# Kernel tuning notes

Hardware: AMD Instinct MI355X
Metric: run time of the kernel (lower is better)

The kernel has to match this reference:

```python
import jax, jax.numpy as jnp
import numpy as np

N = 400_000            # nodes
E = 8_000_000          # edges (avg degree 20)
USER, TOPIC, CAT, GROUP = 200_000, 50_000, 2_000, 30_000
UD, TD, CD, GD = 8, 8, 2, 8   # embedding dims
C = 8                  # input_channels
H = 16                 # hidden layer width
OUT = 1


def setup_inputs() -> dict:
    key = jax.random.key(0)
    ks = jax.random.split(key, 24)

    # node types in {0:user, 1:topic, 2:category, 4:group}
    t = jnp.take(jnp.array([0, 1, 2, 4], dtype=jnp.int32),
                 jax.random.randint(ks[0], (N,), 0, 4))
    # per-type vocab sizes (index 3 is an unused dummy)
    vocab = jnp.array([USER, TOPIC, CAT, 1, GROUP], dtype=jnp.int32)[t]
    i0 = jax.random.randint(ks[1], (N,), 0, 1 << 30) % vocab
    i1 = jax.random.randint(ks[2], (N,), 0, 2)  # known-user flag
    features = jnp.stack([i0, i1, t], axis=1)            # [N, 3] int32
    edges = jax.random.randint(ks[3], (2, E), 0, N)      # [2, E]

    g = lambda k, shape: 0.02 * jax.random.normal(k, shape, dtype=jnp.float32)
    return {
        "edges": edges,
        "features": features,
        "user_emb": g(ks[4], (USER, UD)),
        "known_emb": g(ks[5], (2, UD)),
        "Wu": g(ks[6], (UD, C)), "bu": g(ks[7], (C,)),
        "topic_emb": g(ks[8], (TOPIC, TD)),
        "Wt": g(ks[9], (TD, C)), "bt": g(ks[10], (C,)),
        "cat_emb": g(ks[11], (CAT, CD)),
        "Wc": g(ks[12], (CD, C)), "bc": g(ks[13], (C,)),
        "group_emb": g(ks[14], (GROUP, GD)),
        "Wg": g(ks[15], (GD, C)), "bg": g(ks[16], (C,)),
        "W0": g(ks[17], (C, H)), "b0": g(ks[18], (H,)),
        "W2": g(ks[19], (H, OUT)), "b2": g(ks[20], (OUT,)),
    }


def reference(edges, features, user_emb, known_emb, Wu, bu,
              topic_emb, Wt, bt, cat_emb, Wc, bc,
              group_emb, Wg, bg, W0, b0, W2, b2):
    t = features[:, -1]
    i0 = features[:, 0]
    i1 = features[:, 1]

    # type-specific embedding gather + ReLU + linear projection (safe-indexed)
    u = jax.nn.relu(user_emb[jnp.where(t == 0, i0, 0)]
                    + known_emb[jnp.where(t == 0, i1, 0)]) @ Wu + bu
    tp = jax.nn.relu(topic_emb[jnp.where(t == 1, i0, 0)]) @ Wt + bt
    c = jax.nn.relu(cat_emb[jnp.where(t == 2, i0, 0)]) @ Wc + bc
    g = jax.nn.relu(group_emb[jnp.where(t == 4, i0, 0)]) @ Wg + bg

    tc = t[:, None]
    x = (jnp.where(tc == 0, u, 0.0) + jnp.where(tc == 1, tp, 0.0)
         + jnp.where(tc == 2, c, 0.0) + jnp.where(tc == 4, g, 0.0))  # [N, C]

    n = x.shape[0]
    loops = jnp.arange(n, dtype=edges.dtype)
    row = jnp.concatenate([edges[0], loops])   # source (with self loops)
    col = jnp.concatenate([edges[1], loops])   # target
    deg = jax.ops.segment_sum(jnp.ones_like(col, dtype=x.dtype), col,
                              num_segments=n)
    dinv = jnp.where(deg > 0, jax.lax.rsqrt(deg), 0.0)
    norm = dinv[row] * dinv[col]               # [E+N]

    def gcn_conv(h, W, b):  # PyG GCNConv: D^-1/2 (A+I) D^-1/2 h W + b
        hw = h @ W
        agg = jax.ops.segment_sum(norm[:, None] * hw[row], col, num_segments=n)
        return agg + b

    # original forward applies layers[0] (+ReLU) then layers[-1];
    # the middle GCNConv is skipped and dropout never fires.
    h = jax.nn.relu(gcn_conv(x, W0, b0))
    return gcn_conv(h, W2, b2)
```

## Files before the change

### kernel.cpp

```cpp
#include <hip/hip_runtime.h>

#define SH 10
#define BN 1024
#define CAP 22016
#define TILE 4096
#define MAXB 512
#define NCH 8
#define CSH 16
#define AGG_NB 1024


__device__ __forceinline__ unsigned short f2bf(float f) {
    union { float f; unsigned u; } x; x.f = f;
    unsigned u = x.u + 0x7fffu + ((x.u >> 16) & 1u);
    return (unsigned short)(u >> 16);
}
__device__ __forceinline__ float u2f(unsigned u) {
    union { unsigned u; float f; } x; x.u = u;
    return x.f;
}


__global__ void k_binit(int* __restrict__ bcursor, int pbkt) {
    int b = blockIdx.x * blockDim.x + threadIdx.x;
    if (b < pbkt) bcursor[b] = b * CAP;
}

__global__ void __launch_bounds__(256)
k_part(const int* __restrict__ row, const int* __restrict__ col,
       int* __restrict__ bcursor, unsigned* __restrict__ ebuf, int e) {
    __shared__ int lcnt[MAXB];
    __shared__ int gbase[MAXB];
    int t = threadIdx.x;
    int base = blockIdx.x * TILE;
    for (int j = t; j < MAXB; j += 256) lcnt[j] = 0;
    __syncthreads();
    int myb[16]; int mylpos[16]; unsigned myv[16];
#pragma unroll
    for (int k = 0; k < 16; k++) {
        int i = base + k * 256 + t;
        if (i < e) {
            int r = row[i];
            int c = col[i];
            int b = c >> SH;
            myb[k] = b;
            myv[k] = ((unsigned)r << SH) | (unsigned)(c & (BN - 1));
            mylpos[k] = atomicAdd(&lcnt[b], 1);
        } else {
            myb[k] = -1;
        }
    }
    __syncthreads();
    for (int j = t; j < MAXB; j += 256)
        if (lcnt[j] > 0) gbase[j] = atomicAdd(&bcursor[j], lcnt[j]);
    __syncthreads();
#pragma unroll
    for (int k = 0; k < 16; k++) {
        if (myb[k] >= 0) {
            int idx = gbase[myb[k]] + mylpos[k];
            if (idx < (myb[k] + 1) * CAP) ebuf[idx] = myv[k];
        }
    }
}

__global__ void k_bscan(const int* __restrict__ bcursor, int* __restrict__ bbase, int bkt) {
    __shared__ int sd[256];
    int t = threadIdx.x;
    int i0 = t * 2, i1 = t * 2 + 1;
    int v0 = (i0 < bkt) ? (bcursor[i0] - i0 * CAP) : 0;
    int v1 = (i1 < bkt) ? (bcursor[i1] - i1 * CAP) : 0;
    int s = v0 + v1;
    sd[t] = s; __syncthreads();
    for (int off = 1; off < 256; off <<= 1) {
        int x = (t >= off) ? sd[t - off] : 0;
        __syncthreads();
        sd[t] += x;
        __syncthreads();
    }
    int run = sd[t] - s;
    if (i0 < bkt) bbase[i0] = run;
    if (i1 < bkt) bbase[i1] = run + v0;
}


__global__ void __launch_bounds__(512)
k_scatB(const int* __restrict__ bcursor, const int* __restrict__ bbase,
        const unsigned* __restrict__ ebuf, int* __restrict__ csr,
        int* __restrict__ start, int* __restrict__ cnt, float* __restrict__ dinv,
        uint2* __restrict__ chunkCnt, int n, int bkt) {
    __shared__ int lcnt[BN * NCH];
    __shared__ unsigned stage[CAP];
    __shared__ int sd[512];
    int b = blockIdx.x;
    if (b >= bkt) return;
    int t = threadIdx.x;
    int ebase = b * CAP;
    int len = bcursor[b] - ebase;
    if (len > CAP) len = CAP;
    int cbase = bbase[b];

    for (int j = t; j < BN * NCH; j += 512) lcnt[j] = 0;
    __syncthreads();
    for (int i = t; i < len; i += 512) {
        unsigned vv = ebuf[ebase + i];
        int bin = (int)((vv & (BN - 1)) << 3) | (int)((vv >> SH) >> CSH);
        atomicAdd(&lcnt[bin], 1);
    }
    __syncthreads();
    int v[16]; int s = 0;
#pragma unroll
    for (int k = 0; k < 16; k++) { v[k] = lcnt[t * 16 + k]; s += v[k]; }
    sd[t] = s; __syncthreads();
    for (int off = 1; off < 512; off <<= 1) {
        int x = (t >= off) ? sd[t - off] : 0;
        __syncthreads();
        sd[t] += x;
        __syncthreads();
    }
    int run = sd[t] - s;
    int node0 = b << SH;
#pragma unroll
    for (int nn = 0; nn < 2; nn++) {
        int node = node0 + t * 2 + nn;
        int segbase = run;
        unsigned packA = 0, packB = 0;
        int tot = 0;
#pragma unroll
        for (int k2 = 0; k2 < 8; k2++) {
            int cc = v[nn * 8 + k2];
            lcnt[t * 16 + nn * 8 + k2] = run;
            run += cc; tot += cc;
            unsigned ccs = (unsigned)(cc > 255 ? 255 : cc);
            if (k2 < 4) packA |= ccs << (8 * k2);
            else        packB |= ccs << (8 * (k2 - 4));
        }
        if (node < n) {
            start[node] = cbase + segbase;
            cnt[node] = tot;
            dinv[node] = rsqrtf((float)tot + 1.0f);
            chunkCnt[node] = make_uint2(packA, packB);
        }
    }
    __syncthreads();
    for (int i = t; i < len; i += 512) {
        unsigned vv = ebuf[ebase + i];
        unsigned r = vv >> SH;
        int bin = (int)((vv & (BN - 1)) << 3) | (int)(r >> CSH);
        int p = atomicAdd(&lcnt[bin], 1);
        if (p < CAP) stage[p] = r;
        else csr[cbase + p] = (int)r;
    }
    __syncthreads();
    for (int j = t; j < len; j += 512) csr[cbase + j] = (int)stage[j];
}


__device__ __forceinline__ void matvec8(const float* e, const float* W, const float* b, float* x) {
#pragma unroll
    for (int c = 0; c < 8; c++) x[c] = b[c];
#pragma unroll
    for (int k = 0; k < 8; k++) {
        float r = fmaxf(e[k], 0.0f);
#pragma unroll
        for (int c = 0; c < 8; c++) x[c] = fmaf(r, W[k * 8 + c], x[c]);
    }
}

__global__ void __launch_bounds__(256)
k_node(const int* __restrict__ feat,
       const float* __restrict__ user_emb, const float* __restrict__ known_emb,
       const float* __restrict__ Wu, const float* __restrict__ bu,
       const float* __restrict__ topic_emb, const float* __restrict__ Wt, const float* __restrict__ bt,
       const float* __restrict__ cat_emb, const float* __restrict__ Wc, const float* __restrict__ bc,
       const float* __restrict__ group_emb, const float* __restrict__ Wg, const float* __restrict__ bg,
       const float* __restrict__ W0, const float* __restrict__ dinv,
       unsigned short* __restrict__ yb, int n) {
    __shared__ float sWu[64], sWt[64], sWc[64], sWg[64];
    __shared__ float sbu[8], sbt[8], sbc[8], sbg[8];
    __shared__ float sW0[128];
    int t = threadIdx.x;
    if (t < 64) {
        sWu[t] = Wu[t];
        sWt[t] = Wt[t];
        sWc[t] = (t < 16) ? Wc[t] : 0.0f;
        sWg[t] = Wg[t];
    } else if (t < 192) {
        sW0[t - 64] = W0[t - 64];
    } else if (t < 200) {
        int k = t - 192;
        sbu[k] = bu[k]; sbt[k] = bt[k]; sbc[k] = bc[k]; sbg[k] = bg[k];
    }
    __syncthreads();

    int i = blockIdx.x * blockDim.x + t;
    if (i >= n) return;

    int i0 = feat[3 * i + 0];
    int i1 = feat[3 * i + 1];
    int ty = feat[3 * i + 2];

    float x[8];
    float e[8];
    if (ty == 0) {
        const float4* u = (const float4*)(user_emb + (size_t)i0 * 8);
        const float4* kn = (const float4*)(known_emb + (size_t)i1 * 8);
        float4 a0 = u[0], a1 = u[1], k0 = kn[0], k1 = kn[1];
        e[0] = a0.x + k0.x; e[1] = a0.y + k0.y; e[2] = a0.z + k0.z; e[3] = a0.w + k0.w;
        e[4] = a1.x + k1.x; e[5] = a1.y + k1.y; e[6] = a1.z + k1.z; e[7] = a1.w + k1.w;
        matvec8(e, sWu, sbu, x);
    } else if (ty == 1) {
        const float4* u = (const float4*)(topic_emb + (size_t)i0 * 8);
        float4 a0 = u[0], a1 = u[1];
        e[0] = a0.x; e[1] = a0.y; e[2] = a0.z; e[3] = a0.w;
        e[4] = a1.x; e[5] = a1.y; e[6] = a1.z; e[7] = a1.w;
        matvec8(e, sWt, sbt, x);
    } else if (ty == 2) {
        const float2* u = (const float2*)(cat_emb + (size_t)i0 * 2);
        float2 a = u[0];
        e[0] = a.x; e[1] = a.y;
#pragma unroll
        for (int k = 2; k < 8; k++) e[k] = 0.0f;
        matvec8(e, sWc, sbc, x);
    } else if (ty == 4) {
        const float4* u = (const float4*)(group_emb + (size_t)i0 * 8);
        float4 a0 = u[0], a1 = u[1];
        e[0] = a0.x; e[1] = a0.y; e[2] = a0.z; e[3] = a0.w;
        e[4] = a1.x; e[5] = a1.y; e[6] = a1.z; e[7] = a1.w;
        matvec8(e, sWg, sbg, x);
    } else {
#pragma unroll
        for (int c = 0; c < 8; c++) x[c] = 0.0f;
    }

    float di = dinv[i];
    float yv[16];
#pragma unroll
    for (int h = 0; h < 16; h++) {
        float acc = 0.0f;
#pragma unroll
        for (int c = 0; c < 8; c++) acc = fmaf(x[c], sW0[c * 16 + h], acc);
        yv[h] = di * acc;
    }
    unsigned p[8];
#pragma unroll
    for (int k = 0; k < 8; k++)
        p[k] = (unsigned)f2bf(yv[2 * k]) | ((unsigned)f2bf(yv[2 * k + 1]) << 16);
    uint4* o = (uint4*)(yb + (size_t)i * 16);
    o[0] = make_uint4(p[0], p[1], p[2], p[3]);
    o[1] = make_uint4(p[4], p[5], p[6], p[7]);
}


__device__ __forceinline__ void upadd(uint4 v, float* a) {
    a[0] += u2f(v.x << 16); a[1] += u2f(v.x & 0xffff0000u);
    a[2] += u2f(v.y << 16); a[3] += u2f(v.y & 0xffff0000u);
    a[4] += u2f(v.z << 16); a[5] += u2f(v.z & 0xffff0000u);
    a[6] += u2f(v.w << 16); a[7] += u2f(v.w & 0xffff0000u);
}

__global__ void __launch_bounds__(256, 4)
k_agg1(const int* __restrict__ start, const uint2* __restrict__ chunkCnt,
       const int* __restrict__ csr, const uint4* __restrict__ y4,
       const float* __restrict__ dinv, const float* __restrict__ b0,
       const float* __restrict__ W2, float* __restrict__ y2, int n, int nPerBlk) {
    int t = threadIdx.x;
    int j = t & 1;
    int p = t >> 1;
    int base = blockIdx.x * nPerBlk;
    int end = base + nPerBlk; if (end > n) end = n;

    float acc[4][8];
    int cur[4]; int nd[4];
    unsigned cc0[4], cc1[4];
#pragma unroll
    for (int k = 0; k < 4; k++) {
        int node = base + p + k * 128;
        nd[k] = node;
#pragma unroll
        for (int ch = 0; ch < 8; ch++) acc[k][ch] = 0.0f;
        if (node < end) {
            cur[k] = start[node];
            uint2 cc = chunkCnt[node];
            cc0[k] = cc.x; cc1[k] = cc.y;
            upadd(y4[(size_t)node * 2 + j], acc[k]);
        } else {
            cur[k] = 0; cc0[k] = 0; cc1[k] = 0;
        }
    }

    for (int c = 0; c < 7; c++) {
        int sh = (c & 3) * 8;
#pragma unroll
        for (int k = 0; k < 4; k++) {
            unsigned packed = (c < 4) ? cc0[k] : cc1[k];
            int cc = (int)((packed >> sh) & 255u);
            int s = cur[k];
            cur[k] = s + cc;
            int i = 0;
            for (; i + 2 <= cc; i += 2) {
                int r0 = csr[s + i];
                int r1 = csr[s + i + 1];
                uint4 v0 = y4[(size_t)r0 * 2 + j];
                uint4 v1 = y4[(size_t)r1 * 2 + j];
                upadd(v0, acc[k]); upadd(v1, acc[k]);
            }
            if (i < cc) upadd(y4[(size_t)csr[s + i] * 2 + j], acc[k]);
        }
    }

    float4 bA = ((const float4*)b0)[2 * j];
    float4 bB = ((const float4*)b0)[2 * j + 1];
    float4 wA = ((const float4*)W2)[2 * j];
    float4 wB = ((const float4*)W2)[2 * j + 1];
#pragma unroll
    for (int k = 0; k < 4; k++) {
        if (nd[k] >= end) continue;
        float di = dinv[nd[k]];
        float v = 0.0f;
        v += fmaxf(fmaf(acc[k][0], di, bA.x), 0.0f) * wA.x;
        v += fmaxf(fmaf(acc[k][1], di, bA.y), 0.0f) * wA.y;
        v += fmaxf(fmaf(acc[k][2], di, bA.z), 0.0f) * wA.z;
        v += fmaxf(fmaf(acc[k][3], di, bA.w), 0.0f) * wA.w;
        v += fmaxf(fmaf(acc[k][4], di, bB.x), 0.0f) * wB.x;
        v += fmaxf(fmaf(acc[k][5], di, bB.y), 0.0f) * wB.y;
        v += fmaxf(fmaf(acc[k][6], di, bB.z), 0.0f) * wB.z;
        v += fmaxf(fmaf(acc[k][7], di, bB.w), 0.0f) * wB.w;
        v += __shfl_xor(v, 1);
        if (j == 0) y2[nd[k]] = di * v;
    }
}

__global__ void __launch_bounds__(256)
k_agg2(const int* __restrict__ start, const int* __restrict__ cnt,
       const int* __restrict__ csr, const float* __restrict__ y2,
       const float* __restrict__ dinv, const float* __restrict__ b2,
       float* __restrict__ out, int n) {
    int gid = blockIdx.x * blockDim.x + threadIdx.x;
    int node = gid >> 2;
    int j = gid & 3;
    if (node >= n) return;
    int s = start[node];
    int d = cnt[node];
    float acc = (j == 0) ? y2[node] : 0.0f;
    for (int i = j; i < d; i += 4) acc += y2[csr[s + i]];
    acc += __shfl_xor(acc, 1);
    acc += __shfl_xor(acc, 2);
    if (j == 0) out[node] = fmaf(acc, dinv[node], b2[0]);
}


static inline size_t align_up(size_t v, size_t a) { return (v + a - 1) & ~(a - 1); }

extern "C" void kernel_launch(void* const* d_in, const int* in_sizes, int n_in,
                              void* d_out, int out_size, void* d_ws, size_t ws_size,
                              hipStream_t stream) {
    const int E = in_sizes[0] / 2;
    const int N = in_sizes[1] / 3;

    const int* edges    = (const int*)d_in[0];
    const int* row      = edges;
    const int* col      = edges + E;
    const int* feat     = (const int*)d_in[1];
    const float* user_emb  = (const float*)d_in[2];
    const float* known_emb = (const float*)d_in[3];
    const float* Wu = (const float*)d_in[4];
    const float* bu = (const float*)d_in[5];
    const float* topic_emb = (const float*)d_in[6];
    const float* Wt = (const float*)d_in[7];
    const float* bt = (const float*)d_in[8];
    const float* cat_emb = (const float*)d_in[9];
    const float* Wc = (const float*)d_in[10];
    const float* bc = (const float*)d_in[11];
    const float* group_emb = (const float*)d_in[12];
    const float* Wg = (const float*)d_in[13];
    const float* bg = (const float*)d_in[14];
    const float* W0 = (const float*)d_in[15];
    const float* b0 = (const float*)d_in[16];
    const float* W2 = (const float*)d_in[17];
    const float* b2 = (const float*)d_in[18];

    float* out = (float*)d_out;

    const int BKT  = (N + BN - 1) >> SH;
    const int PBKT = (BKT + 7) & ~7;

    char* w = (char*)d_ws;
    size_t off = 0;
    int* cnt      = (int*)(w + off); off = align_up(off + (size_t)N * 4, 256);
    int* start    = (int*)(w + off); off = align_up(off + (size_t)N * 4, 256);
    float* dinv   = (float*)(w + off); off = align_up(off + (size_t)N * 4, 256);
    float* y2     = (float*)(w + off); off = align_up(off + (size_t)N * 4, 256);
    uint2* chunkCnt = (uint2*)(w + off); off = align_up(off + (size_t)N * 8, 256);
    int* bcursor  = (int*)(w + off); off = align_up(off + MAXB * 4, 256);
    int* bbase    = (int*)(w + off); off = align_up(off + MAXB * 4, 256);
    size_t bigsz = (size_t)BKT * CAP * 4;
    if ((size_t)N * 32 > bigsz) bigsz = (size_t)N * 32;
    unsigned* ebuf      = (unsigned*)(w + off);
    unsigned short* yb  = (unsigned short*)(w + off); off = align_up(off + bigsz, 256);
    int* csr      = (int*)(w + off); off = align_up(off + (size_t)E * 4, 256);
    (void)ws_size;

    int tb = 256;
    int gbN = (N + tb - 1) / tb;
    int ntile = (E + TILE - 1) / TILE;

    k_binit<<<(PBKT + 255) / 256, 256, 0, stream>>>(bcursor, PBKT);
    k_part<<<ntile, tb, 0, stream>>>(row, col, bcursor, ebuf, E);
    k_bscan<<<1, 256, 0, stream>>>(bcursor, bbase, BKT);
    k_scatB<<<BKT, 512, 0, stream>>>(bcursor, bbase, ebuf, csr, start, cnt, dinv,
                                     chunkCnt, N, BKT);
    k_node<<<gbN, tb, 0, stream>>>(feat, user_emb, known_emb, Wu, bu,
                                   topic_emb, Wt, bt, cat_emb, Wc, bc,
                                   group_emb, Wg, bg, W0, dinv, yb, N);
    int nPerBlk = (N + AGG_NB - 1) / AGG_NB;
    k_agg1<<<AGG_NB, tb, 0, stream>>>(start, chunkCnt, csr, (const uint4*)yb,
                                      dinv, b0, W2, y2, N, nPerBlk);
    int gbA24 = ((N * 4) + tb - 1) / tb;
    k_agg2<<<gbA24, tb, 0, stream>>>(start, cnt, csr, y2, dinv, b2, out, N);
}
```

Baseline: 289.3 us.

## Compress CSR source indices to 16-bit offsets within per-chunk ranges

```diff
diff --git a/kernel.cpp b/kernel.cpp
--- a/kernel.cpp
+++ b/kernel.cpp
@@ -7,7 +7,6 @@
 #define MAXB 512
 #define NCH 8
 #define CSH 16
-#define AGG_NB 1024
 
 
 __device__ __forceinline__ unsigned short f2bf(float f) {
@@ -83,13 +82,13 @@
 }
 
 
-__global__ void __launch_bounds__(512)
+__global__ void __launch_bounds__(512, 4)
 k_scatB(const int* __restrict__ bcursor, const int* __restrict__ bbase,
-        const unsigned* __restrict__ ebuf, int* __restrict__ csr,
-        int* __restrict__ start, int* __restrict__ cnt, float* __restrict__ dinv,
+        const unsigned* __restrict__ ebuf, unsigned short* __restrict__ csr16,
+        int* __restrict__ start, float* __restrict__ dinv,
         uint2* __restrict__ chunkCnt, int n, int bkt) {
     __shared__ int lcnt[BN * NCH];
-    __shared__ unsigned stage[CAP];
+    __shared__ unsigned short stage[CAP];
     __shared__ int sd[512];
     int b = blockIdx.x;
     if (b >= bkt) return;
@@ -136,7 +135,6 @@
         }
         if (node < n) {
             start[node] = cbase + segbase;
-            cnt[node] = tot;
             dinv[node] = rsqrtf((float)tot + 1.0f);
             chunkCnt[node] = make_uint2(packA, packB);
         }
@@ -147,11 +145,12 @@
         unsigned r = vv >> SH;
         int bin = (int)((vv & (BN - 1)) << 3) | (int)(r >> CSH);
         int p = atomicAdd(&lcnt[bin], 1);
-        if (p < CAP) stage[p] = r;
-        else csr[cbase + p] = (int)r;
-    }
-    __syncthreads();
-    for (int j = t; j < len; j += 512) csr[cbase + j] = (int)stage[j];
+        unsigned short off16 = (unsigned short)(r & 0xFFFFu);
+        if (p < CAP) stage[p] = off16;
+        else csr16[cbase + p] = off16;
+    }
+    __syncthreads();
+    for (int j = t; j < len; j += 512) csr16[cbase + j] = stage[j];
 }
 
 
@@ -258,93 +257,92 @@
     a[6] += u2f(v.w << 16); a[7] += u2f(v.w & 0xffff0000u);
 }
 
-__global__ void __launch_bounds__(256, 4)
+__global__ void __launch_bounds__(256, 8)
 k_agg1(const int* __restrict__ start, const uint2* __restrict__ chunkCnt,
-       const int* __restrict__ csr, const uint4* __restrict__ y4,
+       const unsigned short* __restrict__ csr16, const uint4* __restrict__ y4,
        const float* __restrict__ dinv, const float* __restrict__ b0,
-       const float* __restrict__ W2, float* __restrict__ y2, int n, int nPerBlk) {
-    int t = threadIdx.x;
-    int j = t & 1;
-    int p = t >> 1;
-    int base = blockIdx.x * nPerBlk;
-    int end = base + nPerBlk; if (end > n) end = n;
-
-    float acc[4][8];
-    int cur[4]; int nd[4];
-    unsigned cc0[4], cc1[4];
-#pragma unroll
-    for (int k = 0; k < 4; k++) {
-        int node = base + p + k * 128;
-        nd[k] = node;
-#pragma unroll
-        for (int ch = 0; ch < 8; ch++) acc[k][ch] = 0.0f;
-        if (node < end) {
-            cur[k] = start[node];
-            uint2 cc = chunkCnt[node];
-            cc0[k] = cc.x; cc1[k] = cc.y;
-            upadd(y4[(size_t)node * 2 + j], acc[k]);
-        } else {
-            cur[k] = 0; cc0[k] = 0; cc1[k] = 0;
-        }
-    }
-
+       const float* __restrict__ W2, float* __restrict__ y2, int n) {
+    int node = blockIdx.x * 256 + threadIdx.x;
+    bool act = node < n;
+    float acc[16];
+#pragma unroll
+    for (int k = 0; k < 16; k++) acc[k] = 0.0f;
+    int cur = 0;
+    uint2 cc = make_uint2(0u, 0u);
+    if (act) {
+        cur = start[node];
+        cc = chunkCnt[node];
+        uint4 s0 = y4[(size_t)node * 2];
+        uint4 s1 = y4[(size_t)node * 2 + 1];
+        upadd(s0, acc); upadd(s1, acc + 8);
+    }
+#pragma unroll
     for (int c = 0; c < 7; c++) {
-        int sh = (c & 3) * 8;
-#pragma unroll
-        for (int k = 0; k < 4; k++) {
-            unsigned packed = (c < 4) ? cc0[k] : cc1[k];
-            int cc = (int)((packed >> sh) & 255u);
-            int s = cur[k];
-            cur[k] = s + cc;
-            int i = 0;
-            for (; i + 2 <= cc; i += 2) {
-                int r0 = csr[s + i];
-                int r1 = csr[s + i + 1];
-                uint4 v0 = y4[(size_t)r0 * 2 + j];
-                uint4 v1 = y4[(size_t)r1 * 2 + j];
-                upadd(v0, acc[k]); upadd(v1, acc[k]);
-            }
-            if (i < cc) upadd(y4[(size_t)csr[s + i] * 2 + j], acc[k]);
-        }
-    }
-
-    float4 bA = ((const float4*)b0)[2 * j];
-    float4 bB = ((const float4*)b0)[2 * j + 1];
-    float4 wA = ((const float4*)W2)[2 * j];
-    float4 wB = ((const float4*)W2)[2 * j + 1];
-#pragma unroll
-    for (int k = 0; k < 4; k++) {
-        if (nd[k] >= end) continue;
-        float di = dinv[nd[k]];
+        unsigned packed = (c < 4) ? cc.x : cc.y;
+        int k = (int)((packed >> ((c & 3) * 8)) & 255u);
+        int s = cur; cur += k;
+        size_t hi = ((size_t)c << (CSH + 1));
+        int i = 0;
+        for (; i + 2 <= k; i += 2) {
+            int o0 = csr16[s + i];
+            int o1 = csr16[s + i + 1];
+            size_t r0 = hi + ((size_t)o0 << 1);
+            size_t r1 = hi + ((size_t)o1 << 1);
+            uint4 va0 = y4[r0], va1 = y4[r0 + 1];
+            uint4 vb0 = y4[r1], vb1 = y4[r1 + 1];
+            upadd(va0, acc); upadd(va1, acc + 8);
+            upadd(vb0, acc); upadd(vb1, acc + 8);
+        }
+        if (i < k) {
+            int o = csr16[s + i];
+            size_t r = hi + ((size_t)o << 1);
+            upadd(y4[r], acc); upadd(y4[r + 1], acc + 8);
+        }
+    }
+    if (act) {
+        float di = dinv[node];
         float v = 0.0f;
-        v += fmaxf(fmaf(acc[k][0], di, bA.x), 0.0f) * wA.x;
-        v += fmaxf(fmaf(acc[k][1], di, bA.y), 0.0f) * wA.y;
-        v += fmaxf(fmaf(acc[k][2], di, bA.z), 0.0f) * wA.z;
-        v += fmaxf(fmaf(acc[k][3], di, bA.w), 0.0f) * wA.w;
-        v += fmaxf(fmaf(acc[k][4], di, bB.x), 0.0f) * wB.x;
-        v += fmaxf(fmaf(acc[k][5], di, bB.y), 0.0f) * wB.y;
-        v += fmaxf(fmaf(acc[k][6], di, bB.z), 0.0f) * wB.z;
-        v += fmaxf(fmaf(acc[k][7], di, bB.w), 0.0f) * wB.w;
-        v += __shfl_xor(v, 1);
-        if (j == 0) y2[nd[k]] = di * v;
+#pragma unroll
+        for (int k = 0; k < 16; k++)
+            v += fmaxf(fmaf(acc[k], di, b0[k]), 0.0f) * W2[k];
+        y2[node] = di * v;
     }
 }
 
 __global__ void __launch_bounds__(256)
-k_agg2(const int* __restrict__ start, const int* __restrict__ cnt,
-       const int* __restrict__ csr, const float* __restrict__ y2,
+k_agg2(const int* __restrict__ start, const uint2* __restrict__ chunkCnt,
+       const unsigned short* __restrict__ csr16, const float* __restrict__ y2,
        const float* __restrict__ dinv, const float* __restrict__ b2,
        float* __restrict__ out, int n) {
     int gid = blockIdx.x * blockDim.x + threadIdx.x;
-    int node = gid >> 2;
-    int j = gid & 3;
+    int node = gid >> 1;
+    int j = gid & 1;
     if (node >= n) return;
+    uint2 cc = chunkCnt[node];
     int s = start[node];
-    int d = cnt[node];
-    float acc = (j == 0) ? y2[node] : 0.0f;
-    for (int i = j; i < d; i += 4) acc += y2[csr[s + i]];
+    float acc;
+    int c0, c1;
+    if (j == 0) {
+        acc = y2[node]; c0 = 0; c1 = 4;
+    } else {
+        s += (int)((cc.x & 255u) + ((cc.x >> 8) & 255u) + ((cc.x >> 16) & 255u) + (cc.x >> 24));
+        acc = 0.0f; c0 = 4; c1 = 7;
+    }
+    for (int c = c0; c < c1; c++) {
+        unsigned packed = (c < 4) ? cc.x : cc.y;
+        int k = (int)((packed >> ((c & 3) * 8)) & 255u);
+        int base = c << CSH;
+        int i = 0;
+        for (; i + 2 <= k; i += 2) {
+            int o0 = csr16[s + i];
+            int o1 = csr16[s + i + 1];
+            acc += y2[base + o0];
+            acc += y2[base + o1];
+        }
+        if (i < k) acc += y2[base + csr16[s + i]];
+        s += k;
+    }
     acc += __shfl_xor(acc, 1);
-    acc += __shfl_xor(acc, 2);
     if (j == 0) out[node] = fmaf(acc, dinv[node], b2[0]);
 }
 
@@ -386,7 +384,6 @@
 
     char* w = (char*)d_ws;
     size_t off = 0;
-    int* cnt      = (int*)(w + off); off = align_up(off + (size_t)N * 4, 256);
     int* start    = (int*)(w + off); off = align_up(off + (size_t)N * 4, 256);
     float* dinv   = (float*)(w + off); off = align_up(off + (size_t)N * 4, 256);
     float* y2     = (float*)(w + off); off = align_up(off + (size_t)N * 4, 256);
@@ -397,7 +394,7 @@
     if ((size_t)N * 32 > bigsz) bigsz = (size_t)N * 32;
     unsigned* ebuf      = (unsigned*)(w + off);
     unsigned short* yb  = (unsigned short*)(w + off); off = align_up(off + bigsz, 256);
-    int* csr      = (int*)(w + off); off = align_up(off + (size_t)E * 4, 256);
+    unsigned short* csr16 = (unsigned short*)(w + off); off = align_up(off + (size_t)E * 2, 256);
     (void)ws_size;
 
     int tb = 256;
@@ -407,14 +404,13 @@
     k_binit<<<(PBKT + 255) / 256, 256, 0, stream>>>(bcursor, PBKT);
     k_part<<<ntile, tb, 0, stream>>>(row, col, bcursor, ebuf, E);
     k_bscan<<<1, 256, 0, stream>>>(bcursor, bbase, BKT);
-    k_scatB<<<BKT, 512, 0, stream>>>(bcursor, bbase, ebuf, csr, start, cnt, dinv,
+    k_scatB<<<BKT, 512, 0, stream>>>(bcursor, bbase, ebuf, csr16, start, dinv,
                                      chunkCnt, N, BKT);
     k_node<<<gbN, tb, 0, stream>>>(feat, user_emb, known_emb, Wu, bu,
                                    topic_emb, Wt, bt, cat_emb, Wc, bc,
                                    group_emb, Wg, bg, W0, dinv, yb, N);
-    int nPerBlk = (N + AGG_NB - 1) / AGG_NB;
-    k_agg1<<<AGG_NB, tb, 0, stream>>>(start, chunkCnt, csr, (const uint4*)yb,
-                                      dinv, b0, W2, y2, N, nPerBlk);
-    int gbA24 = ((N * 4) + tb - 1) / tb;
-    k_agg2<<<gbA24, tb, 0, stream>>>(start, cnt, csr, y2, dinv, b2, out, N);
-}
+    k_agg1<<<gbN, tb, 0, stream>>>(start, chunkCnt, csr16, (const uint4*)yb,
+                                   dinv, b0, W2, y2, N);
+    int gbA22 = ((N * 2) + tb - 1) / tb;
+    k_agg2<<<gbA22, tb, 0, stream>>>(start, chunkCnt, csr16, y2, dinv, b2, out, N);
+}
```

Result: no change. 289.0 us (-0.1%).

## Compress CSR to 16-bit offsets within source-chunk bins, add nontemporal hints

Applied to the files above, without the earlier changes.

```diff
diff --git a/kernel.cpp b/kernel.cpp
--- a/kernel.cpp
+++ b/kernel.cpp
@@ -58,7 +58,8 @@
     for (int k = 0; k < 16; k++) {
         if (myb[k] >= 0) {
             int idx = gbase[myb[k]] + mylpos[k];
-            if (idx < (myb[k] + 1) * CAP) ebuf[idx] = myv[k];
+            if (idx < (myb[k] + 1) * CAP)
+                __builtin_nontemporal_store(myv[k], &ebuf[idx]);
         }
     }
 }
@@ -83,13 +84,13 @@
 }
 
 
-__global__ void __launch_bounds__(512)
+__global__ void __launch_bounds__(512, 4)
 k_scatB(const int* __restrict__ bcursor, const int* __restrict__ bbase,
-        const unsigned* __restrict__ ebuf, int* __restrict__ csr,
-        int* __restrict__ start, int* __restrict__ cnt, float* __restrict__ dinv,
+        const unsigned* __restrict__ ebuf, unsigned short* __restrict__ csr16,
+        int* __restrict__ start, float* __restrict__ dinv,
         uint2* __restrict__ chunkCnt, int n, int bkt) {
     __shared__ int lcnt[BN * NCH];
-    __shared__ unsigned stage[CAP];
+    __shared__ unsigned short stage[CAP];
     __shared__ int sd[512];
     int b = blockIdx.x;
     if (b >= bkt) return;
@@ -102,7 +103,7 @@
     for (int j = t; j < BN * NCH; j += 512) lcnt[j] = 0;
     __syncthreads();
     for (int i = t; i < len; i += 512) {
-        unsigned vv = ebuf[ebase + i];
+        unsigned vv = __builtin_nontemporal_load(&ebuf[ebase + i]);
         int bin = (int)((vv & (BN - 1)) << 3) | (int)((vv >> SH) >> CSH);
         atomicAdd(&lcnt[bin], 1);
     }
@@ -136,22 +137,23 @@
         }
         if (node < n) {
             start[node] = cbase + segbase;
-            cnt[node] = tot;
             dinv[node] = rsqrtf((float)tot + 1.0f);
             chunkCnt[node] = make_uint2(packA, packB);
         }
     }
     __syncthreads();
     for (int i = t; i < len; i += 512) {
-        unsigned vv = ebuf[ebase + i];
+        unsigned vv = __builtin_nontemporal_load(&ebuf[ebase + i]);
         unsigned r = vv >> SH;
         int bin = (int)((vv & (BN - 1)) << 3) | (int)(r >> CSH);
         int p = atomicAdd(&lcnt[bin], 1);
-        if (p < CAP) stage[p] = r;
-        else csr[cbase + p] = (int)r;
-    }
-    __syncthreads();
-    for (int j = t; j < len; j += 512) csr[cbase + j] = (int)stage[j];
+        unsigned short off16 = (unsigned short)(r & 0xFFFFu);
+        if (p < CAP) stage[p] = off16;
+        else csr16[cbase + p] = off16;
+    }
+    __syncthreads();
+    for (int j = t; j < len; j += 512)
+        __builtin_nontemporal_store(stage[j], &csr16[cbase + j]);
 }
 
 
@@ -260,7 +262,7 @@
 
 __global__ void __launch_bounds__(256, 4)
 k_agg1(const int* __restrict__ start, const uint2* __restrict__ chunkCnt,
-       const int* __restrict__ csr, const uint4* __restrict__ y4,
+       const unsigned short* __restrict__ csr16, const uint4* __restrict__ y4,
        const float* __restrict__ dinv, const float* __restrict__ b0,
        const float* __restrict__ W2, float* __restrict__ y2, int n, int nPerBlk) {
     int t = threadIdx.x;
@@ -290,6 +292,7 @@
 
     for (int c = 0; c < 7; c++) {
         int sh = (c & 3) * 8;
+        size_t hi = ((size_t)c << (CSH + 1)) + j;
 #pragma unroll
         for (int k = 0; k < 4; k++) {
             unsigned packed = (c < 4) ? cc0[k] : cc1[k];
@@ -298,13 +301,16 @@
             cur[k] = s + cc;
             int i = 0;
             for (; i + 2 <= cc; i += 2) {
-                int r0 = csr[s + i];
-                int r1 = csr[s + i + 1];
-                uint4 v0 = y4[(size_t)r0 * 2 + j];
-                uint4 v1 = y4[(size_t)r1 * 2 + j];
+                int o0 = __builtin_nontemporal_load(&csr16[s + i]);
+                int o1 = __builtin_nontemporal_load(&csr16[s + i + 1]);
+                uint4 v0 = y4[hi + ((size_t)o0 << 1)];
+                uint4 v1 = y4[hi + ((size_t)o1 << 1)];
                 upadd(v0, acc[k]); upadd(v1, acc[k]);
             }
-            if (i < cc) upadd(y4[(size_t)csr[s + i] * 2 + j], acc[k]);
+            if (i < cc) {
+                int o = __builtin_nontemporal_load(&csr16[s + i]);
+                upadd(y4[hi + ((size_t)o << 1)], acc[k]);
+            }
         }
     }
 
@@ -326,25 +332,44 @@
         v += fmaxf(fmaf(acc[k][6], di, bB.z), 0.0f) * wB.z;
         v += fmaxf(fmaf(acc[k][7], di, bB.w), 0.0f) * wB.w;
         v += __shfl_xor(v, 1);
-        if (j == 0) y2[nd[k]] = di * v;
+        if (j == 0) __builtin_nontemporal_store(di * v, &y2[nd[k]]);
     }
 }
 
 __global__ void __launch_bounds__(256)
-k_agg2(const int* __restrict__ start, const int* __restrict__ cnt,
-       const int* __restrict__ csr, const float* __restrict__ y2,
+k_agg2(const int* __restrict__ start, const uint2* __restrict__ chunkCnt,
+       const unsigned short* __restrict__ csr16, const float* __restrict__ y2,
        const float* __restrict__ dinv, const float* __restrict__ b2,
        float* __restrict__ out, int n) {
     int gid = blockIdx.x * blockDim.x + threadIdx.x;
-    int node = gid >> 2;
-    int j = gid & 3;
+    int node = gid >> 1;
+    int j = gid & 1;
     if (node >= n) return;
+    uint2 cc = chunkCnt[node];
     int s = start[node];
-    int d = cnt[node];
-    float acc = (j == 0) ? y2[node] : 0.0f;
-    for (int i = j; i < d; i += 4) acc += y2[csr[s + i]];
+    float acc;
+    int c0, c1;
+    if (j == 0) {
+        acc = y2[node]; c0 = 0; c1 = 4;
+    } else {
+        s += (int)((cc.x & 255u) + ((cc.x >> 8) & 255u) + ((cc.x >> 16) & 255u) + (cc.x >> 24));
+        acc = 0.0f; c0 = 4; c1 = 7;
+    }
+    for (int c = c0; c < c1; c++) {
+        unsigned packed = (c < 4) ? cc.x : cc.y;
+        int k = (int)((packed >> ((c & 3) * 8)) & 255u);
+        int base = c << CSH;
+        int i = 0;
+        for (; i + 2 <= k; i += 2) {
+            int o0 = __builtin_nontemporal_load(&csr16[s + i]);
+            int o1 = __builtin_nontemporal_load(&csr16[s + i + 1]);
+            acc += y2[base + o0];
+            acc += y2[base + o1];
+        }
+        if (i < k) acc += y2[base + __builtin_nontemporal_load(&csr16[s + i])];
+        s += k;
+    }
     acc += __shfl_xor(acc, 1);
-    acc += __shfl_xor(acc, 2);
     if (j == 0) out[node] = fmaf(acc, dinv[node], b2[0]);
 }
 
@@ -386,7 +411,6 @@
 
     char* w = (char*)d_ws;
     size_t off = 0;
-    int* cnt      = (int*)(w + off); off = align_up(off + (size_t)N * 4, 256);
     int* start    = (int*)(w + off); off = align_up(off + (size_t)N * 4, 256);
     float* dinv   = (float*)(w + off); off = align_up(off + (size_t)N * 4, 256);
     float* y2     = (float*)(w + off); off = align_up(off + (size_t)N * 4, 256);
@@ -397,7 +421,7 @@
     if ((size_t)N * 32 > bigsz) bigsz = (size_t)N * 32;
     unsigned* ebuf      = (unsigned*)(w + off);
     unsigned short* yb  = (unsigned short*)(w + off); off = align_up(off + bigsz, 256);
-    int* csr      = (int*)(w + off); off = align_up(off + (size_t)E * 4, 256);
+    unsigned short* csr16 = (unsigned short*)(w + off); off = align_up(off + (size_t)E * 2, 256);
     (void)ws_size;
 
     int tb = 256;
@@ -407,14 +431,14 @@
     k_binit<<<(PBKT + 255) / 256, 256, 0, stream>>>(bcursor, PBKT);
     k_part<<<ntile, tb, 0, stream>>>(row, col, bcursor, ebuf, E);
     k_bscan<<<1, 256, 0, stream>>>(bcursor, bbase, BKT);
-    k_scatB<<<BKT, 512, 0, stream>>>(bcursor, bbase, ebuf, csr, start, cnt, dinv,
+    k_scatB<<<BKT, 512, 0, stream>>>(bcursor, bbase, ebuf, csr16, start, dinv,
                                      chunkCnt, N, BKT);
     k_node<<<gbN, tb, 0, stream>>>(feat, user_emb, known_emb, Wu, bu,
                                    topic_emb, Wt, bt, cat_emb, Wc, bc,
                                    group_emb, Wg, bg, W0, dinv, yb, N);
     int nPerBlk = (N + AGG_NB - 1) / AGG_NB;
-    k_agg1<<<AGG_NB, tb, 0, stream>>>(start, chunkCnt, csr, (const uint4*)yb,
+    k_agg1<<<AGG_NB, tb, 0, stream>>>(start, chunkCnt, csr16, (const uint4*)yb,
                                       dinv, b0, W2, y2, N, nPerBlk);
-    int gbA24 = ((N * 4) + tb - 1) / tb;
-    k_agg2<<<gbA24, tb, 0, stream>>>(start, cnt, csr, y2, dinv, b2, out, N);
-}
+    int gbA22 = ((N * 2) + tb - 1) / tb;
+    k_agg2<<<gbA22, tb, 0, stream>>>(start, chunkCnt, csr16, y2, dinv, b2, out, N);
+}
```

After: 594.0 us. 105% more time.
